# Kernel tuning notes

Measured on AMD Instinct MI355X. Metric: run time of the kernel, lower is better.

Reference implementation:

```python
import jax, jax.numpy as jnp
import numpy as np

B, L, N, D = 32, 12, 512, 128
H = 4            # num attention heads
FK = 256         # forecast fc out dim
OUT_STEPS = 12   # seq_length
GAP = 1
MAX_PE = 64
LN_EPS = 1e-5


def _pe_table():
    pos = np.arange(MAX_PE)[:, None].astype(np.float32)
    div = np.exp(np.arange(0, D, 2).astype(np.float32) * (-np.log(10000.0) / D))
    pe = np.zeros((MAX_PE, 1, D), np.float32)
    pe[:, 0, 0::2] = np.sin(pos * div)
    pe[:, 0, 1::2] = np.cos(pos * div)
    return jnp.asarray(pe)


def setup_inputs() -> dict:
    key = jax.random.key(0)
    ks = jax.random.split(key, 16)
    def rn(k, shape, scale=0.05):
        return jax.random.normal(k, shape, dtype=jnp.float32) * scale
    return {
        "X": rn(ks[0], (B, L, N, D), 1.0),
        "gru_w_ih": rn(ks[1], (3 * D, D)),
        "gru_w_hh": rn(ks[2], (3 * D, D)),
        "gru_b_ih": rn(ks[3], (3 * D,)),
        "gru_b_hh": rn(ks[4], (3 * D,)),
        "attn_in_w": rn(ks[5], (3 * D, D)),
        "attn_in_b": rn(ks[6], (3 * D,)),
        "attn_out_w": rn(ks[7], (D, D)),
        "attn_out_b": rn(ks[8], (D,)),
        "backcast_w": rn(ks[9], (D, D)),
        "backcast_b": rn(ks[10], (D,)),
        "forecast_w": rn(ks[11], (FK, D)),
        "forecast_b": rn(ks[12], (FK,)),
        "ln_gamma": jnp.ones((D,), jnp.float32),
        "ln_beta": jnp.zeros((D,), jnp.float32),
    }


def reference(X, gru_w_ih, gru_w_hh, gru_b_ih, gru_b_hh,
              attn_in_w, attn_in_b, attn_out_w, attn_out_b,
              backcast_w, backcast_b, forecast_w, forecast_b,
              ln_gamma, ln_beta):
    pe = _pe_table()

    def gru(x, h):  # (BN,D),(BN,D) -> (BN,D)  torch.nn.GRUCell math (r,z,n order)
        gi = x @ gru_w_ih.T + gru_b_ih
        gh = h @ gru_w_hh.T + gru_b_hh
        ir, iz, inn = jnp.split(gi, 3, axis=-1)
        hr, hz, hn = jnp.split(gh, 3, axis=-1)
        r = jax.nn.sigmoid(ir + hr)
        z = jax.nn.sigmoid(iz + hz)
        n = jnp.tanh(inn + r * hn)
        return (1.0 - z) * n + z * h

    def mha(q_in, kv):  # seq-first (Lq,BN,D),(Lk,BN,D) -> (Lq,BN,D)
        wq, wk, wv = jnp.split(attn_in_w, 3, axis=0)
        bq, bk, bv = jnp.split(attn_in_b, 3, axis=0)
        hd = D // H
        q = (q_in @ wq.T + bq).reshape(q_in.shape[0], -1, H, hd)
        k = (kv @ wk.T + bk).reshape(kv.shape[0], -1, H, hd)
        v = (kv @ wv.T + bv).reshape(kv.shape[0], -1, H, hd)
        scores = jnp.einsum('qbhd,kbhd->bhqk', q, k) / jnp.sqrt(jnp.float32(hd))
        attn = jax.nn.softmax(scores, axis=-1)
        out = jnp.einsum('bhqk,kbhd->qbhd', attn, v).reshape(q_in.shape[0], -1, D)
        return out @ attn_out_w.T + attn_out_b

    # --- RNNLayer: per-node GRU over L steps (dropout in eval = identity) ---
    Xs = X.transpose(0, 2, 1, 3).reshape(B * N, L, D).transpose(1, 0, 2)  # (L,BN,D)
    h0 = jnp.zeros((B * N, D), X.dtype)
    def step(h, xt):
        hn = gru(xt, h)
        return hn, hn
    _, rnn_raw = jax.lax.scan(step, h0, Xs)  # (L,BN,D)

    # --- pos encoder (first=True) + self-attention ---
    rnn_pe = rnn_raw + pe[:L]
    Z0 = mha(rnn_pe, rnn_pe)  # (L,BN,D)

    # --- InhForecast: growing-KV decode loop (PE re-added each iteration, as in source) ---
    RNN_H = rnn_raw
    predict = [Z0[-1:]]
    for _ in range(OUT_STEPS // GAP - 1):
        g = gru(predict[-1][0], RNN_H[-1])[None]          # (1,BN,D)
        RNN_H = jnp.concatenate([RNN_H, g], axis=0)
        RNN_H = RNN_H + pe[:RNN_H.shape[0]]               # pe(RNN_H) each step
        predict.append(mha(g, RNN_H))                     # (1,BN,D)
    pred = jnp.concatenate(predict, axis=0)               # (T,BN,D)
    pred = pred.reshape(-1, B, N, D).transpose(1, 0, 2, 3)  # (B,T,N,D)
    forecast = pred @ forecast_w.T + forecast_b           # (B,T,N,FK)

    # --- backcast + ResidualDecomp: LN(X - relu(backcast)) ---
    Zb = Z0.reshape(L, B, N, D).transpose(1, 0, 2, 3)     # (B,L,N,D)
    back = Zb @ backcast_w.T + backcast_b
    u = X - jax.nn.relu(back)
    mu = jnp.mean(u, axis=-1, keepdims=True)
    var = jnp.var(u, axis=-1, keepdims=True)
    res = (u - mu) / jnp.sqrt(var + LN_EPS) * ln_gamma + ln_beta
    return (res, forecast)
```

## Files before the change

kernel.cpp:

```cpp
#include <hip/hip_runtime.h>
#include <hip/hip_bf16.h>
#include <math.h>

#define BB 32
#define LL 12
#define NN 512
#define DD 128
#define BN 16384
#define HH 4
#define TT 12
#define FKK 256
#define NSLOT 23

__device__ __forceinline__ float selv(const float4& v, int j) {
    return (j == 0) ? v.x : ((j == 1) ? v.y : ((j == 2) ? v.z : v.w));
}

__device__ __forceinline__ void stage64(float (*sT)[68], const float* base,
                                        long outer, int row0, int tid,
                                        const float* addrow) {
    int sm  = tid & 7;
    int skg = tid >> 3;
    int sk  = skg << 2;
#pragma unroll
    for (int i = 0; i < 8; ++i) {
        int m   = sm + i * 8;
        int row = row0 + m;
        const float4 v = *(const float4*)(base + (long)(row >> 9) * outer +
                                          (long)(row & 511) * 128 + sk);
#pragma unroll
        for (int jj = 0; jj < 4; ++jj) {
            int j = (jj + skg) & 3;
            float val = selv(v, j);
            if (addrow) val += addrow[sk + j];
            sT[sk + j][m] = val;
        }
    }
}

__device__ __forceinline__ void mm128(const float (*aT)[68], const float (*bT)[68],
                                      int tm4, int tn4, float (&acc)[4][4]) {
#pragma unroll 8
    for (int k = 0; k < 128; ++k) {
        const float4 a = *(const float4*)&aT[k][tm4];
        const float4 b = *(const float4*)&bT[k][tn4];
        acc[0][0] += a.x * b.x; acc[0][1] += a.x * b.y; acc[0][2] += a.x * b.z; acc[0][3] += a.x * b.w;
        acc[1][0] += a.y * b.x; acc[1][1] += a.y * b.y; acc[1][2] += a.y * b.z; acc[1][3] += a.y * b.w;
        acc[2][0] += a.z * b.x; acc[2][1] += a.z * b.y; acc[2][2] += a.z * b.z; acc[2][3] += a.z * b.w;
        acc[3][0] += a.w * b.x; acc[3][1] += a.w * b.y; acc[3][2] += a.w * b.z; acc[3][3] += a.w * b.w;
    }
}

__global__ __launch_bounds__(128) void pe_init(const float* __restrict__ Wqkv,
                                               float* __restrict__ pe,
                                               float* __restrict__ peq,
                                               float* __restrict__ pek,
                                               float* __restrict__ pev) {
    int p = blockIdx.x, d = threadIdx.x;
    __shared__ float per[128];
    int i2 = (d >> 1) << 1;
    float dv  = expf(-(float)i2 * 0.0719557841560639f);
    float arg = (float)p * dv;
    per[d] = (d & 1) ? cosf(arg) : sinf(arg);
    __syncthreads();
    pe[p * 128 + d] = per[d];
    float sq = 0.f, sk = 0.f, sv = 0.f;
    for (int k = 0; k < 128; ++k) {
        float pv = per[k];
        sq += pv * Wqkv[d * 128 + k];
        sk += pv * Wqkv[(128 + d) * 128 + k];
        sv += pv * Wqkv[(256 + d) * 128 + k];
    }
    peq[p * 128 + d] = sq;
    pek[p * 128 + d] = sk;
    pev[p * 128 + d] = sv;
}

__global__ __launch_bounds__(256) void gemm_k128(
    const float* __restrict__ A, long a_outer,
    const float* __restrict__ W, const float* __restrict__ bias,
    float* __restrict__ C0, float* __restrict__ C1, float* __restrict__ C2,
    long c_outer, int c_inner) {
    __shared__ float aT[128][68];
    __shared__ float wT[128][68];
    int tid  = threadIdx.x;
    int mblk = blockIdx.x * 64;
    int nblk = blockIdx.y * 64;
    stage64(aT, A, a_outer, mblk, tid, nullptr);
    stage64(wT, W, 0, nblk, tid, nullptr);
    __syncthreads();
    float acc[4][4] = {};
    int tn4 = (tid & 15) << 2;
    int tm4 = (tid >> 4) << 2;
    mm128(aT, wT, tm4, tn4, acc);
    int cb = nblk + tn4;
    const float4 b4 = *(const float4*)(bias + cb);
    float* Cp = (cb >= 256) ? C2 : ((cb >= 128) ? C1 : C0);
    int cc = cb & 127;
#pragma unroll
    for (int im = 0; im < 4; ++im) {
        int row = mblk + tm4 + im;
        float4 o = make_float4(acc[im][0] + b4.x, acc[im][1] + b4.y,
                               acc[im][2] + b4.z, acc[im][3] + b4.w);
        *(float4*)(Cp + (long)(row >> 9) * c_outer + (long)(row & 511) * c_inner + cc) = o;
    }
}

template <bool HZERO, bool HADD>
__global__ __launch_bounds__(256) void gru_step(
    const float* __restrict__ Xb, long x_outer,
    const float* __restrict__ Hb, const float* __restrict__ hadd,
    const float* __restrict__ Wih, const float* __restrict__ Whh,
    const float* __restrict__ bih, const float* __restrict__ bhh,
    float* __restrict__ Hout) {
    __shared__ float xT[128][68];
    __shared__ float hT[128][68];
    __shared__ float wT[128][68];
    int tid  = threadIdx.x;
    int mblk = blockIdx.x * 64;
    int dblk = blockIdx.y * 64;
    stage64(xT, Xb, x_outer, mblk, tid, nullptr);
    if (!HZERO) stage64(hT, Hb, 65536, mblk, tid, HADD ? hadd : nullptr);
    int tn4 = (tid & 15) << 2;
    int tm4 = (tid >> 4) << 2;
    float acc[3][2][4][4] = {};
#pragma unroll
    for (int g = 0; g < 3; ++g) {
        __syncthreads();
        stage64(wT, Wih, 0, g * 128 + dblk, tid, nullptr);
        __syncthreads();
        mm128(xT, wT, tm4, tn4, acc[g][0]);
        if (!HZERO) {
            __syncthreads();
            stage64(wT, Whh, 0, g * 128 + dblk, tid, nullptr);
            __syncthreads();
            mm128(hT, wT, tm4, tn4, acc[g][1]);
        }
    }
#define GRU_COMB(JD, DEST)                                                        \
    {                                                                             \
        int d = dblk + tn4 + JD;                                                  \
        float hprev = HZERO ? 0.f : hT[d][tm4 + im];                              \
        float rr = acc[0][0][im][JD] + bih[d] + bhh[d] +                          \
                   (HZERO ? 0.f : acc[0][1][im][JD]);                             \
        float r = 1.f / (1.f + expf(-rr));                                        \
        float zz = acc[1][0][im][JD] + bih[128 + d] + bhh[128 + d] +              \
                   (HZERO ? 0.f : acc[1][1][im][JD]);                             \
        float z = 1.f / (1.f + expf(-zz));                                        \
        float hn = bhh[256 + d] + (HZERO ? 0.f : acc[2][1][im][JD]);              \
        float n = tanhf(acc[2][0][im][JD] + bih[256 + d] + r * hn);               \
        DEST = (1.f - z) * n + z * hprev;                                         \
    }
#pragma unroll
    for (int im = 0; im < 4; ++im) {
        int row = mblk + tm4 + im;
        float o0, o1, o2, o3;
        GRU_COMB(0, o0) GRU_COMB(1, o1) GRU_COMB(2, o2) GRU_COMB(3, o3)
        *(float4*)(Hout + (long)row * 128 + dblk + tn4) = make_float4(o0, o1, o2, o3);
    }
#undef GRU_COMB
}

__global__ __launch_bounds__(256) void attn_z0(
    const float* Q, const float* __restrict__ K, const float* __restrict__ V,
    const float* __restrict__ peq, const float* __restrict__ pek,
    const float* __restrict__ pev, float* AO) {
    int bn = blockIdx.x, tid = threadIdx.x;
    __shared__ float Qs[12][132], Ks[12][132], Vs[12][132];
    __shared__ float sc[4][12][12];
    for (int idx = tid; idx < 12 * 128; idx += 256) {
        int t = idx >> 7, d = idx & 127;
        long g = ((long)(t * BN + bn) << 7) + d;
        Qs[t][d] = Q[g] + peq[t * 128 + d];
        Ks[t][d] = K[g] + pek[t * 128 + d];
        Vs[t][d] = V[g] + pev[t * 128 + d];
    }
    __syncthreads();
    for (int idx = tid; idx < 576; idx += 256) {
        int h = idx / 144, r = idx - h * 144;
        int q = r / 12, k = r - (r / 12) * 12;
        float s = 0.f;
#pragma unroll
        for (int d = 0; d < 32; ++d) s += Qs[q][h * 32 + d] * Ks[k][h * 32 + d];
        sc[h][q][k] = s * 0.17677669529663687f;
    }
    __syncthreads();
    if (tid < 48) {
        int h = tid / 12, q = tid - (tid / 12) * 12;
        float mx = sc[h][q][0];
#pragma unroll
        for (int k = 1; k < 12; ++k) mx = fmaxf(mx, sc[h][q][k]);
        float sum = 0.f;
#pragma unroll
        for (int k = 0; k < 12; ++k) { float e = expf(sc[h][q][k] - mx); sc[h][q][k] = e; sum += e; }
        float inv = 1.f / sum;
#pragma unroll
        for (int k = 0; k < 12; ++k) sc[h][q][k] *= inv;
    }
    __syncthreads();
    for (int idx = tid; idx < 1536; idx += 256) {
        int q = idx >> 7, d = idx & 127, h = d >> 5;
        float s = 0.f;
#pragma unroll
        for (int k = 0; k < 12; ++k) s += sc[h][q][k] * Vs[k][d];
        AO[((long)(q * BN + bn) << 7) + d] = s;
    }
}

__global__ __launch_bounds__(256) void attn_dec(
    const float* __restrict__ Qg, const float* __restrict__ K,
    const float* __restrict__ V, const float* __restrict__ pek,
    const float* __restrict__ pev, float* __restrict__ AOd, int NK, int iter) {
    int bn = blockIdx.x, tid = threadIdx.x;
    __shared__ float qs[128];
    __shared__ float Ks[NSLOT][132], Vs[NSLOT][132];
    __shared__ float sc[4][NSLOT];
    if (tid < 128) qs[tid] = Qg[((long)bn << 7) + tid];
    for (int idx = tid; idx < NK * 128; idx += 256) {
        int j = idx >> 7, d = idx & 127;
        int ci = iter + 1, cj = 13 + iter - j;
        float c = (float)(ci < cj ? ci : cj);
        long g = ((long)(j * BN + bn) << 7) + d;
        Ks[j][d] = K[g] + c * pek[j * 128 + d];
        Vs[j][d] = V[g] + c * pev[j * 128 + d];
    }
    __syncthreads();
    for (int idx = tid; idx < 4 * NK; idx += 256) {
        int h = idx / NK, j = idx - h * NK;
        float s = 0.f;
#pragma unroll
        for (int d = 0; d < 32; ++d) s += qs[h * 32 + d] * Ks[j][h * 32 + d];
        sc[h][j] = s * 0.17677669529663687f;
    }
    __syncthreads();
    if (tid < 4) {
        float mx = -1e30f;
        for (int j = 0; j < NK; ++j) mx = fmaxf(mx, sc[tid][j]);
        float sum = 0.f;
        for (int j = 0; j < NK; ++j) { float e = expf(sc[tid][j] - mx); sc[tid][j] = e; sum += e; }
        float inv = 1.f / sum;
        for (int j = 0; j < NK; ++j) sc[tid][j] *= inv;
    }
    __syncthreads();
    if (tid < 128) {
        int h = tid >> 5;
        float s = 0.f;
        for (int j = 0; j < NK; ++j) s += sc[h][j] * Vs[j][tid];
        AOd[((long)bn << 7) + tid] = s;
    }
}

__global__ __launch_bounds__(256) void backcast_ln(
    const float* __restrict__ BACK, const float* __restrict__ X,
    const float* __restrict__ gamma, const float* __restrict__ beta,
    float* __restrict__ OUT) {
    int tid = threadIdx.x, lane = tid & 63, wv = tid >> 6;
    int row = blockIdx.x * 4 + wv;
    int t = row >> 14, bn = row & 16383;
    int b = bn >> 9, n = bn & 511;
    long xoff = ((long)((b * 12 + t) * 512 + n) << 7) + lane * 2;
    float2 bk = *(const float2*)(BACK + ((long)row << 7) + lane * 2);
    float2 xv = *(const float2*)(X + xoff);
    float u0 = xv.x - fmaxf(bk.x, 0.f);
    float u1 = xv.y - fmaxf(bk.y, 0.f);
    float s = u0 + u1, sq = u0 * u0 + u1 * u1;
#pragma unroll
    for (int o = 32; o > 0; o >>= 1) { s += __shfl_xor(s, o); sq += __shfl_xor(sq, o); }
    float mu  = s * (1.f / 128.f);
    float var = sq * (1.f / 128.f) - mu * mu;
    float rs  = 1.f / sqrtf(var + 1e-5f);
    int d = lane * 2;
    float2 o;
    o.x = (u0 - mu) * rs * gamma[d] + beta[d];
    o.y = (u1 - mu) * rs * gamma[d + 1] + beta[d + 1];
    *(float2*)(OUT + xoff) = o;
}

extern "C" void kernel_launch(void* const* d_in, const int* in_sizes, int n_in,
                              void* d_out, int out_size, void* d_ws, size_t ws_size,
                              hipStream_t stream) {
    const float* X    = (const float*)d_in[0];
    const float* Wih  = (const float*)d_in[1];
    const float* Whh  = (const float*)d_in[2];
    const float* bih  = (const float*)d_in[3];
    const float* bhh  = (const float*)d_in[4];
    const float* Wqkv = (const float*)d_in[5];
    const float* bqkv = (const float*)d_in[6];
    const float* Wo   = (const float*)d_in[7];
    const float* bo   = (const float*)d_in[8];
    const float* Wb   = (const float*)d_in[9];
    const float* bb   = (const float*)d_in[10];
    const float* Wf   = (const float*)d_in[11];
    const float* bf   = (const float*)d_in[12];
    const float* gam  = (const float*)d_in[13];
    const float* bet  = (const float*)d_in[14];
    float* res = (float*)d_out;
    float* fc  = (float*)d_out + (long)BB * LL * NN * DD;

    float* w   = (float*)d_ws;
    float* pe  = w; w += 24 * 128;
    float* peq = w; w += 24 * 128;
    float* pek = w; w += 24 * 128;
    float* pev = w; w += 24 * 128;
    float* RNN = w; w += (long)LL * BN * DD;
    float* Kb  = w; w += (long)NSLOT * BN * DD;
    float* Vb  = w; w += (long)NSLOT * BN * DD;
    float* QA  = w; w += (long)LL * BN * DD;
    float* Z0  = w; w += (long)LL * BN * DD;
    float* Qg  = w; w += (long)BN * DD;
    float* AOd = w; w += (long)BN * DD;
    float* G   = w; w += (long)2 * BN * DD;
    float* P   = w; w += (long)2 * BN * DD;

    const long CONT = 65536;
    const long FOUT = (long)TT * NN * FKK;

    pe_init<<<23, 128, 0, stream>>>(Wqkv, pe, peq, pek, pev);

    for (int t = 0; t < 12; ++t) {
        dim3 gr(BN / 64, 2);
        const float* xb = X + (long)t * NN * DD;
        if (t == 0)
            gru_step<true, false><<<gr, 256, 0, stream>>>(
                xb, (long)LL * NN * DD, nullptr, nullptr, Wih, Whh, bih, bhh, RNN);
        else
            gru_step<false, false><<<gr, 256, 0, stream>>>(
                xb, (long)LL * NN * DD, RNN + (long)(t - 1) * BN * DD, nullptr,
                Wih, Whh, bih, bhh, RNN + (long)t * BN * DD);
    }

    gemm_k128<<<dim3(LL * BN / 64, 6), 256, 0, stream>>>(
        RNN, CONT, Wqkv, bqkv, QA, Kb, Vb, CONT, 128);
    attn_z0<<<BN, 256, 0, stream>>>(QA, Kb, Vb, peq, pek, pev, QA);
    gemm_k128<<<dim3(LL * BN / 64, 2), 256, 0, stream>>>(
        QA, CONT, Wo, bo, Z0, nullptr, nullptr, CONT, 128);

    gemm_k128<<<dim3(LL * BN / 64, 2), 256, 0, stream>>>(
        Z0, CONT, Wb, bb, QA, nullptr, nullptr, CONT, 128);
    backcast_ln<<<LL * BN / 4, 256, 0, stream>>>(QA, X, gam, bet, res);

    gemm_k128<<<dim3(BN / 64, 4), 256, 0, stream>>>(
        Z0 + (long)11 * BN * DD, CONT, Wf, bf, fc, fc + 128, nullptr, FOUT, FKK);

    for (int i = 0; i < 11; ++i) {
        float* g        = G + (long)(i & 1) * BN * DD;
        const float* gp = G + (long)((i - 1) & 1) * BN * DD;
        float* p        = P + (long)(i & 1) * BN * DD;
        const float* pp = P + (long)((i - 1) & 1) * BN * DD;
        const float* xsrc = (i == 0) ? Z0 + (long)11 * BN * DD : pp;
        dim3 gr(BN / 64, 2);
        if (i == 0)
            gru_step<false, false><<<gr, 256, 0, stream>>>(
                xsrc, CONT, RNN + (long)11 * BN * DD, nullptr, Wih, Whh, bih, bhh, g);
        else
            gru_step<false, true><<<gr, 256, 0, stream>>>(
                xsrc, CONT, gp, pe + (11 + i) * 128, Wih, Whh, bih, bhh, g);
        gemm_k128<<<dim3(BN / 64, 6), 256, 0, stream>>>(
            g, CONT, Wqkv, bqkv, Qg, Kb + (long)(12 + i) * BN * DD,
            Vb + (long)(12 + i) * BN * DD, CONT, 128);
        attn_dec<<<BN, 256, 0, stream>>>(Qg, Kb, Vb, pek, pev, AOd, 13 + i, i);
        gemm_k128<<<dim3(BN / 64, 2), 256, 0, stream>>>(
            AOd, CONT, Wo, bo, p, nullptr, nullptr, CONT, 128);
        gemm_k128<<<dim3(BN / 64, 4), 256, 0, stream>>>(
            p, CONT, Wf, bf, fc + (long)(i + 1) * NN * FKK,
            fc + (long)(i + 1) * NN * FKK + 128, nullptr, FOUT, FKK);
    }
}
```

Baseline: 6.315 ms.

## Replace FP32 SIMT GEMMs with split-bf16x3 MFMA kernels for GRU and projections

Moves all dense GEMMs (GRU cell, QKV, output, backcast and forecast projections) from shared-memory FP32 FMA tiling to bf16 MFMA instructions. Each fp32 value is split into three bf16 parts and multiplied with six MFMAs to keep near-fp32 accuracy. Weights are pre-split once by a new prep kernel, and activations are split in registers. Fragments are loaded directly from global memory with no LDS staging, which trades LDS reuse for more global traffic. The PE table init also switches to double-precision transcendentals.

```diff
diff --git a/kernel.cpp b/kernel.cpp
--- a/kernel.cpp
+++ b/kernel.cpp
@@ -12,42 +12,59 @@
 #define FKK 256
 #define NSLOT 23
 
-__device__ __forceinline__ float selv(const float4& v, int j) {
-    return (j == 0) ? v.x : ((j == 1) ? v.y : ((j == 2) ? v.z : v.w));
-}
-
-__device__ __forceinline__ void stage64(float (*sT)[68], const float* base,
-                                        long outer, int row0, int tid,
-                                        const float* addrow) {
-    int sm  = tid & 7;
-    int skg = tid >> 3;
-    int sk  = skg << 2;
-#pragma unroll
-    for (int i = 0; i < 8; ++i) {
-        int m   = sm + i * 8;
-        int row = row0 + m;
-        const float4 v = *(const float4*)(base + (long)(row >> 9) * outer +
-                                          (long)(row & 511) * 128 + sk);
-#pragma unroll
-        for (int jj = 0; jj < 4; ++jj) {
-            int j = (jj + skg) & 3;
-            float val = selv(v, j);
-            if (addrow) val += addrow[sk + j];
-            sT[sk + j][m] = val;
-        }
-    }
-}
-
-__device__ __forceinline__ void mm128(const float (*aT)[68], const float (*bT)[68],
-                                      int tm4, int tn4, float (&acc)[4][4]) {
-#pragma unroll 8
-    for (int k = 0; k < 128; ++k) {
-        const float4 a = *(const float4*)&aT[k][tm4];
-        const float4 b = *(const float4*)&bT[k][tn4];
-        acc[0][0] += a.x * b.x; acc[0][1] += a.x * b.y; acc[0][2] += a.x * b.z; acc[0][3] += a.x * b.w;
-        acc[1][0] += a.y * b.x; acc[1][1] += a.y * b.y; acc[1][2] += a.y * b.z; acc[1][3] += a.y * b.w;
-        acc[2][0] += a.z * b.x; acc[2][1] += a.z * b.y; acc[2][2] += a.z * b.z; acc[2][3] += a.z * b.w;
-        acc[3][0] += a.w * b.x; acc[3][1] += a.w * b.y; acc[3][2] += a.w * b.z; acc[3][3] += a.w * b.w;
+typedef __attribute__((ext_vector_type(8))) short short8v;
+typedef __attribute__((ext_vector_type(4))) float f32x4;
+
+__device__ __forceinline__ void split3(float f, short& s0, short& s1, short& s2) {
+    unsigned u = __builtin_bit_cast(unsigned, f);
+    s0 = (short)(u >> 16);
+    float f0 = __builtin_bit_cast(float, u & 0xFFFF0000u);
+    float r1 = f - f0;
+    unsigned u1 = __builtin_bit_cast(unsigned, r1);
+    s1 = (short)(u1 >> 16);
+    float f1 = __builtin_bit_cast(float, u1 & 0xFFFF0000u);
+    s2 = (short)(__builtin_bit_cast(unsigned, r1 - f1) >> 16);
+}
+
+#define MFMA(A, B, C) __builtin_amdgcn_mfma_f32_16x16x32_bf16(A, B, C, 0, 0, 0)
+
+__device__ __forceinline__ f32x4 mfma6(const short8v& a0, const short8v& a1,
+                                       const short8v& a2, const short8v& w0,
+                                       const short8v& w1, const short8v& w2,
+                                       f32x4 acc) {
+    acc = MFMA(a0, w2, acc);
+    acc = MFMA(a2, w0, acc);
+    acc = MFMA(a1, w1, acc);
+    acc = MFMA(a0, w1, acc);
+    acc = MFMA(a1, w0, acc);
+    acc = MFMA(a0, w0, acc);
+    return acc;
+}
+
+__device__ __forceinline__ void load_frags(const float* __restrict__ base, long outer,
+                                           long rowbase, int l15, int lg,
+                                           const float* __restrict__ addv,
+                                           short8v (&F0)[4], short8v (&F1)[4],
+                                           short8v (&F2)[4]) {
+    long row = rowbase + l15;
+    const float* ap = base + (row >> 9) * outer + (row & 511) * 128 + lg * 8;
+#pragma unroll
+    for (int s = 0; s < 4; ++s) {
+        float4 v0 = *(const float4*)(ap + s * 32);
+        float4 v1 = *(const float4*)(ap + s * 32 + 4);
+        if (addv) {
+            const float4 a0 = *(const float4*)(addv + lg * 8 + s * 32);
+            const float4 a1 = *(const float4*)(addv + lg * 8 + s * 32 + 4);
+            v0.x += a0.x; v0.y += a0.y; v0.z += a0.z; v0.w += a0.w;
+            v1.x += a1.x; v1.y += a1.y; v1.z += a1.z; v1.w += a1.w;
+        }
+        float f[8] = {v0.x, v0.y, v0.z, v0.w, v1.x, v1.y, v1.z, v1.w};
+#pragma unroll
+        for (int e = 0; e < 8; ++e) {
+            short t0, t1, t2;
+            split3(f[e], t0, t1, t2);
+            F0[s][e] = t0; F1[s][e] = t1; F2[s][e] = t2;
+        }
     }
 }
 
@@ -59,9 +76,11 @@
     int p = blockIdx.x, d = threadIdx.x;
     __shared__ float per[128];
     int i2 = (d >> 1) << 1;
-    float dv  = expf(-(float)i2 * 0.0719557841560639f);
-    float arg = (float)p * dv;
-    per[d] = (d & 1) ? cosf(arg) : sinf(arg);
+    float sf = (float)(-::log(10000.0) / 128.0);
+    float x = (float)i2 * sf;
+    float div = (float)::exp((double)x);
+    float arg = (float)p * div;
+    per[d] = (d & 1) ? (float)::cos((double)arg) : (float)::sin((double)arg);
     __syncthreads();
     pe[p * 128 + d] = per[d];
     float sq = 0.f, sk = 0.f, sv = 0.f;
@@ -76,89 +95,151 @@
     pev[p * 128 + d] = sv;
 }
 
-__global__ __launch_bounds__(256) void gemm_k128(
+__global__ __launch_bounds__(256) void wprep(
+    const float* __restrict__ Wih, const float* __restrict__ Whh,
+    const float* __restrict__ Wqkv, const float* __restrict__ Wo,
+    const float* __restrict__ Wb, const float* __restrict__ Wf,
+    short* __restrict__ W0, short* __restrict__ W1, short* __restrict__ W2) {
+    int idx = blockIdx.x * 256 + threadIdx.x;
+    int row = idx >> 7;
+    const float* src; int r0;
+    if (row < 384) { src = Wih; r0 = 0; }
+    else if (row < 768) { src = Whh; r0 = 384; }
+    else if (row < 1152) { src = Wqkv; r0 = 768; }
+    else if (row < 1280) { src = Wo; r0 = 1152; }
+    else if (row < 1408) { src = Wb; r0 = 1280; }
+    else { src = Wf; r0 = 1408; }
+    float f = src[idx - (r0 << 7)];
+    short t0, t1, t2;
+    split3(f, t0, t1, t2);
+    W0[idx] = t0; W1[idx] = t1; W2[idx] = t2;
+}
+
+template <int NC, int CFPB>
+__global__ __launch_bounds__(256) void mfma_gemm(
     const float* __restrict__ A, long a_outer,
-    const float* __restrict__ W, const float* __restrict__ bias,
+    const short* __restrict__ W0, const short* __restrict__ W1,
+    const short* __restrict__ W2, const float* __restrict__ bias,
     float* __restrict__ C0, float* __restrict__ C1, float* __restrict__ C2,
-    long c_outer, int c_inner) {
-    __shared__ float aT[128][68];
-    __shared__ float wT[128][68];
-    int tid  = threadIdx.x;
-    int mblk = blockIdx.x * 64;
-    int nblk = blockIdx.y * 64;
-    stage64(aT, A, a_outer, mblk, tid, nullptr);
-    stage64(wT, W, 0, nblk, tid, nullptr);
-    __syncthreads();
-    float acc[4][4] = {};
-    int tn4 = (tid & 15) << 2;
-    int tm4 = (tid >> 4) << 2;
-    mm128(aT, wT, tm4, tn4, acc);
-    int cb = nblk + tn4;
-    const float4 b4 = *(const float4*)(bias + cb);
-    float* Cp = (cb >= 256) ? C2 : ((cb >= 128) ? C1 : C0);
-    int cc = cb & 127;
-#pragma unroll
-    for (int im = 0; im < 4; ++im) {
-        int row = mblk + tm4 + im;
-        float4 o = make_float4(acc[im][0] + b4.x, acc[im][1] + b4.y,
-                               acc[im][2] + b4.z, acc[im][3] + b4.w);
-        *(float4*)(Cp + (long)(row >> 9) * c_outer + (long)(row & 511) * c_inner + cc) = o;
+    long c_outer, long c_inner) {
+    int tid = threadIdx.x, lane = tid & 63, wid = tid >> 6;
+    int l15 = lane & 15, lg = lane >> 4;
+    long rowbase = (long)blockIdx.x * 64 + wid * 16;
+    short8v A0[4], A1[4], A2[4];
+    load_frags(A, a_outer, rowbase, l15, lg, nullptr, A0, A1, A2);
+    int cfbeg = blockIdx.y * CFPB;
+#pragma unroll 2
+    for (int cf = 0; cf < CFPB; ++cf) {
+        int colg = (cfbeg + cf) * 16;
+        long woff = (long)(colg + l15) * 128 + lg * 8;
+        f32x4 acc = {0.f, 0.f, 0.f, 0.f};
+#pragma unroll
+        for (int s = 0; s < 4; ++s) {
+            short8v w0 = *(const short8v*)(W0 + woff + s * 32);
+            short8v w1 = *(const short8v*)(W1 + woff + s * 32);
+            short8v w2 = *(const short8v*)(W2 + woff + s * 32);
+            acc = mfma6(A0[s], A1[s], A2[s], w0, w1, w2, acc);
+        }
+        float b = bias[colg + l15];
+        float* Cp; int cc = colg + l15;
+        if (NC > 256 && colg >= 256) { Cp = C2; cc -= 256; }
+        else if (NC > 128 && colg >= 128) { Cp = C1; cc -= 128; }
+        else { Cp = C0; }
+#pragma unroll
+        for (int r = 0; r < 4; ++r) {
+            long row = rowbase + 4 * lg + r;
+            Cp[(row >> 9) * c_outer + (row & 511) * c_inner + cc] = acc[r] + b;
+        }
     }
 }
 
 template <bool HZERO, bool HADD>
-__global__ __launch_bounds__(256) void gru_step(
+__global__ __launch_bounds__(256) void mfma_gru(
     const float* __restrict__ Xb, long x_outer,
     const float* __restrict__ Hb, const float* __restrict__ hadd,
-    const float* __restrict__ Wih, const float* __restrict__ Whh,
+    const short* __restrict__ Wi0, const short* __restrict__ Wi1,
+    const short* __restrict__ Wi2,
+    const short* __restrict__ Wh0, const short* __restrict__ Wh1,
+    const short* __restrict__ Wh2,
     const float* __restrict__ bih, const float* __restrict__ bhh,
     float* __restrict__ Hout) {
-    __shared__ float xT[128][68];
-    __shared__ float hT[128][68];
-    __shared__ float wT[128][68];
-    int tid  = threadIdx.x;
-    int mblk = blockIdx.x * 64;
-    int dblk = blockIdx.y * 64;
-    stage64(xT, Xb, x_outer, mblk, tid, nullptr);
-    if (!HZERO) stage64(hT, Hb, 65536, mblk, tid, HADD ? hadd : nullptr);
-    int tn4 = (tid & 15) << 2;
-    int tm4 = (tid >> 4) << 2;
-    float acc[3][2][4][4] = {};
-#pragma unroll
-    for (int g = 0; g < 3; ++g) {
-        __syncthreads();
-        stage64(wT, Wih, 0, g * 128 + dblk, tid, nullptr);
-        __syncthreads();
-        mm128(xT, wT, tm4, tn4, acc[g][0]);
-        if (!HZERO) {
-            __syncthreads();
-            stage64(wT, Whh, 0, g * 128 + dblk, tid, nullptr);
-            __syncthreads();
-            mm128(hT, wT, tm4, tn4, acc[g][1]);
-        }
-    }
-#define GRU_COMB(JD, DEST)                                                        \
-    {                                                                             \
-        int d = dblk + tn4 + JD;                                                  \
-        float hprev = HZERO ? 0.f : hT[d][tm4 + im];                              \
-        float rr = acc[0][0][im][JD] + bih[d] + bhh[d] +                          \
-                   (HZERO ? 0.f : acc[0][1][im][JD]);                             \
-        float r = 1.f / (1.f + expf(-rr));                                        \
-        float zz = acc[1][0][im][JD] + bih[128 + d] + bhh[128 + d] +              \
-                   (HZERO ? 0.f : acc[1][1][im][JD]);                             \
-        float z = 1.f / (1.f + expf(-zz));                                        \
-        float hn = bhh[256 + d] + (HZERO ? 0.f : acc[2][1][im][JD]);              \
-        float n = tanhf(acc[2][0][im][JD] + bih[256 + d] + r * hn);               \
-        DEST = (1.f - z) * n + z * hprev;                                         \
-    }
-#pragma unroll
-    for (int im = 0; im < 4; ++im) {
-        int row = mblk + tm4 + im;
-        float o0, o1, o2, o3;
-        GRU_COMB(0, o0) GRU_COMB(1, o1) GRU_COMB(2, o2) GRU_COMB(3, o3)
-        *(float4*)(Hout + (long)row * 128 + dblk + tn4) = make_float4(o0, o1, o2, o3);
-    }
-#undef GRU_COMB
+    int tid = threadIdx.x, lane = tid & 63, wid = tid >> 6;
+    int l15 = lane & 15, lg = lane >> 4;
+    long rowbase = (long)blockIdx.x * 64 + wid * 16;
+    short8v X0[4], X1[4], X2[4];
+    short8v H0[4], H1[4], H2[4];
+    load_frags(Xb, x_outer, rowbase, l15, lg, nullptr, X0, X1, X2);
+    if (!HZERO)
+        load_frags(Hb, 65536, rowbase, l15, lg, HADD ? hadd : nullptr, H0, H1, H2);
+#pragma unroll 1
+    for (int cg = 0; cg < 8; ++cg) {
+        int d = cg * 16 + l15;
+        f32x4 ar = {0.f, 0.f, 0.f, 0.f};
+        f32x4 az = {0.f, 0.f, 0.f, 0.f};
+        f32x4 an = {0.f, 0.f, 0.f, 0.f};
+        f32x4 ahn = {0.f, 0.f, 0.f, 0.f};
+        long wr = (long)d * 128 + lg * 8;
+        long wz = (long)(128 + d) * 128 + lg * 8;
+        long wn = (long)(256 + d) * 128 + lg * 8;
+#pragma unroll
+        for (int s = 0; s < 4; ++s) {
+            int so = s * 32;
+            {
+                short8v w0 = *(const short8v*)(Wi0 + wr + so);
+                short8v w1 = *(const short8v*)(Wi1 + wr + so);
+                short8v w2 = *(const short8v*)(Wi2 + wr + so);
+                ar = mfma6(X0[s], X1[s], X2[s], w0, w1, w2, ar);
+            }
+            {
+                short8v w0 = *(const short8v*)(Wi0 + wz + so);
+                short8v w1 = *(const short8v*)(Wi1 + wz + so);
+                short8v w2 = *(const short8v*)(Wi2 + wz + so);
+                az = mfma6(X0[s], X1[s], X2[s], w0, w1, w2, az);
+            }
+            {
+                short8v w0 = *(const short8v*)(Wi0 + wn + so);
+                short8v w1 = *(const short8v*)(Wi1 + wn + so);
+                short8v w2 = *(const short8v*)(Wi2 + wn + so);
+                an = mfma6(X0[s], X1[s], X2[s], w0, w1, w2, an);
+            }
+            if (!HZERO) {
+                {
+                    short8v w0 = *(const short8v*)(Wh0 + wr + so);
+                    short8v w1 = *(const short8v*)(Wh1 + wr + so);
+                    short8v w2 = *(const short8v*)(Wh2 + wr + so);
+                    ar = mfma6(H0[s], H1[s], H2[s], w0, w1, w2, ar);
+                }
+                {
+                    short8v w0 = *(const short8v*)(Wh0 + wz + so);
+                    short8v w1 = *(const short8v*)(Wh1 + wz + so);
+                    short8v w2 = *(const short8v*)(Wh2 + wz + so);
+                    az = mfma6(H0[s], H1[s], H2[s], w0, w1, w2, az);
+                }
+                {
+                    short8v w0 = *(const short8v*)(Wh0 + wn + so);
+                    short8v w1 = *(const short8v*)(Wh1 + wn + so);
+                    short8v w2 = *(const short8v*)(Wh2 + wn + so);
+                    ahn = mfma6(H0[s], H1[s], H2[s], w0, w1, w2, ahn);
+                }
+            }
+        }
+        float bi0 = bih[d], bi1 = bih[128 + d], bi2 = bih[256 + d];
+        float bh0 = bhh[d], bh1 = bhh[128 + d], bh2 = bhh[256 + d];
+#pragma unroll
+        for (int r = 0; r < 4; ++r) {
+            long row = rowbase + 4 * lg + r;
+            float hp = 0.f;
+            if (!HZERO) {
+                hp = Hb[row * 128 + d];
+                if (HADD) hp += hadd[d];
+            }
+            float rr = 1.f / (1.f + expf(-(ar[r] + bi0 + bh0)));
+            float zz = 1.f / (1.f + expf(-(az[r] + bi1 + bh1)));
+            float hn = bh2 + (HZERO ? 0.f : ahn[r]);
+            float nn = tanhf(an[r] + bi2 + rr * hn);
+            Hout[row * 128 + d] = (1.f - zz) * nn + zz * hp;
+        }
+    }
 }
 
 __global__ __launch_bounds__(256) void attn_z0(
@@ -266,9 +347,9 @@
     float s = u0 + u1, sq = u0 * u0 + u1 * u1;
 #pragma unroll
     for (int o = 32; o > 0; o >>= 1) { s += __shfl_xor(s, o); sq += __shfl_xor(sq, o); }
-    float mu  = s * (1.f / 128.f);
+    float mu = s * (1.f / 128.f);
     float var = sq * (1.f / 128.f) - mu * mu;
-    float rs  = 1.f / sqrtf(var + 1e-5f);
+    float rs = 1.f / sqrtf(var + 1e-5f);
     int d = lane * 2;
     float2 o;
     o.x = (u0 - mu) * rs * gamma[d] + beta[d];
@@ -297,7 +378,11 @@
     float* res = (float*)d_out;
     float* fc  = (float*)d_out + (long)BB * LL * NN * DD;
 
-    float* w   = (float*)d_ws;
+    const long WROWS = 1664;
+    short* Wsp0 = (short*)d_ws;
+    short* Wsp1 = Wsp0 + WROWS * 128;
+    short* Wsp2 = Wsp1 + WROWS * 128;
+    float* w   = (float*)(Wsp2 + WROWS * 128);
     float* pe  = w; w += 24 * 128;
     float* peq = w; w += 24 * 128;
     float* pek = w; w += 24 * 128;
@@ -312,35 +397,45 @@
     float* G   = w; w += (long)2 * BN * DD;
     float* P   = w; w += (long)2 * BN * DD;
 
+    const short* wih0 = Wsp0,        * wih1 = Wsp1,        * wih2 = Wsp2;
+    const short* whh0 = Wsp0 + 384 * 128, * whh1 = Wsp1 + 384 * 128, * whh2 = Wsp2 + 384 * 128;
+    const short* wqk0 = Wsp0 + 768 * 128, * wqk1 = Wsp1 + 768 * 128, * wqk2 = Wsp2 + 768 * 128;
+    const short* wo0  = Wsp0 + 1152 * 128, * wo1 = Wsp1 + 1152 * 128, * wo2 = Wsp2 + 1152 * 128;
+    const short* wb0  = Wsp0 + 1280 * 128, * wb1 = Wsp1 + 1280 * 128, * wb2 = Wsp2 + 1280 * 128;
+    const short* wf0  = Wsp0 + 1408 * 128, * wf1 = Wsp1 + 1408 * 128, * wf2 = Wsp2 + 1408 * 128;
+
     const long CONT = 65536;
     const long FOUT = (long)TT * NN * FKK;
 
-    pe_init<<<23, 128, 0, stream>>>(Wqkv, pe, peq, pek, pev);
+    pe_init<<<24, 128, 0, stream>>>(Wqkv, pe, peq, pek, pev);
+    wprep<<<832, 256, 0, stream>>>(Wih, Whh, Wqkv, Wo, Wb, Wf, Wsp0, Wsp1, Wsp2);
 
     for (int t = 0; t < 12; ++t) {
-        dim3 gr(BN / 64, 2);
         const float* xb = X + (long)t * NN * DD;
         if (t == 0)
-            gru_step<true, false><<<gr, 256, 0, stream>>>(
-                xb, (long)LL * NN * DD, nullptr, nullptr, Wih, Whh, bih, bhh, RNN);
+            mfma_gru<true, false><<<256, 256, 0, stream>>>(
+                xb, (long)LL * NN * DD, nullptr, nullptr,
+                wih0, wih1, wih2, whh0, whh1, whh2, bih, bhh, RNN);
         else
-            gru_step<false, false><<<gr, 256, 0, stream>>>(
+            mfma_gru<false, false><<<256, 256, 0, stream>>>(
                 xb, (long)LL * NN * DD, RNN + (long)(t - 1) * BN * DD, nullptr,
-                Wih, Whh, bih, bhh, RNN + (long)t * BN * DD);
-    }
-
-    gemm_k128<<<dim3(LL * BN / 64, 6), 256, 0, stream>>>(
-        RNN, CONT, Wqkv, bqkv, QA, Kb, Vb, CONT, 128);
+                wih0, wih1, wih2, whh0, whh1, whh2, bih, bhh,
+                RNN + (long)t * BN * DD);
+    }
+
+    mfma_gemm<384, 24><<<dim3(3072, 1), 256, 0, stream>>>(
+        RNN, CONT, wqk0, wqk1, wqk2, bqkv, QA, Kb, Vb, CONT, 128);
     attn_z0<<<BN, 256, 0, stream>>>(QA, Kb, Vb, peq, pek, pev, QA);
-    gemm_k128<<<dim3(LL * BN / 64, 2), 256, 0, stream>>>(
-        QA, CONT, Wo, bo, Z0, nullptr, nullptr, CONT, 128);
-
-    gemm_k128<<<dim3(LL * BN / 64, 2), 256, 0, stream>>>(
-        Z0, CONT, Wb, bb, QA, nullptr, nullptr, CONT, 128);
+    mfma_gemm<128, 8><<<dim3(3072, 1), 256, 0, stream>>>(
+        QA, CONT, wo0, wo1, wo2, bo, Z0, nullptr, nullptr, CONT, 128);
+
+    mfma_gemm<128, 8><<<dim3(3072, 1), 256, 0, stream>>>(
+        Z0, CONT, wb0, wb1, wb2, bb, QA, nullptr, nullptr, CONT, 128);
     backcast_ln<<<LL * BN / 4, 256, 0, stream>>>(QA, X, gam, bet, res);
 
-    gemm_k128<<<dim3(BN / 64, 4), 256, 0, stream>>>(
-        Z0 + (long)11 * BN * DD, CONT, Wf, bf, fc, fc + 128, nullptr, FOUT, FKK);
+    mfma_gemm<256, 8><<<dim3(256, 2), 256, 0, stream>>>(
+        Z0 + (long)11 * BN * DD, CONT, wf0, wf1, wf2, bf, fc, fc + 128, nullptr,
+        FOUT, FKK);
 
     for (int i = 0; i < 11; ++i) {
         float* g        = G + (long)(i & 1) * BN * DD;
@@ -348,21 +443,22 @@
         float* p        = P + (long)(i & 1) * BN * DD;
         const float* pp = P + (long)((i - 1) & 1) * BN * DD;
         const float* xsrc = (i == 0) ? Z0 + (long)11 * BN * DD : pp;
-        dim3 gr(BN / 64, 2);
         if (i == 0)
-            gru_step<false, false><<<gr, 256, 0, stream>>>(
-                xsrc, CONT, RNN + (long)11 * BN * DD, nullptr, Wih, Whh, bih, bhh, g);
+            mfma_gru<false, false><<<256, 256, 0, stream>>>(
+                xsrc, CONT, RNN + (long)11 * BN * DD, nullptr,
+                wih0, wih1, wih2, whh0, whh1, whh2, bih, bhh, g);
         else
-            gru_step<false, true><<<gr, 256, 0, stream>>>(
-                xsrc, CONT, gp, pe + (11 + i) * 128, Wih, Whh, bih, bhh, g);
-        gemm_k128<<<dim3(BN / 64, 6), 256, 0, stream>>>(
-            g, CONT, Wqkv, bqkv, Qg, Kb + (long)(12 + i) * BN * DD,
+            mfma_gru<false, true><<<256, 256, 0, stream>>>(
+                xsrc, CONT, gp, pe + (11 + i) * 128,
+                wih0, wih1, wih2, whh0, whh1, whh2, bih, bhh, g);
+        mfma_gemm<384, 12><<<dim3(256, 2), 256, 0, stream>>>(
+            g, CONT, wqk0, wqk1, wqk2, bqkv, Qg, Kb + (long)(12 + i) * BN * DD,
             Vb + (long)(12 + i) * BN * DD, CONT, 128);
         attn_dec<<<BN, 256, 0, stream>>>(Qg, Kb, Vb, pek, pev, AOd, 13 + i, i);
-        gemm_k128<<<dim3(BN / 64, 2), 256, 0, stream>>>(
-            AOd, CONT, Wo, bo, p, nullptr, nullptr, CONT, 128);
-        gemm_k128<<<dim3(BN / 64, 4), 256, 0, stream>>>(
-            p, CONT, Wf, bf, fc + (long)(i + 1) * NN * FKK,
+        mfma_gemm<128, 4><<<dim3(256, 2), 256, 0, stream>>>(
+            AOd, CONT, wo0, wo1, wo2, bo, p, nullptr, nullptr, CONT, 128);
+        mfma_gemm<256, 8><<<dim3(256, 2), 256, 0, stream>>>(
+            p, CONT, wf0, wf1, wf2, bf, fc + (long)(i + 1) * NN * FKK,
             fc + (long)(i + 1) * NN * FKK + 128, nullptr, FOUT, FKK);
     }
 }
```

Measured after the change: 5.224 ms. 17.3% less time.
